# Optimization experiments

Measured on AMD Instinct MI355X. Metric: run time of the kernel, lower is better.

Reference implementation:

```python
import jax, jax.numpy as jnp
import numpy as np

DIM, EMBED, HEADS = 768, 512, 8
HEAD_DIM = EMBED // HEADS


def setup_inputs() -> dict:
    key = jax.random.key(0)
    ks = jax.random.split(key, 11)
    B, S = 4, 2048
    s = 0.02
    return {
        "query": jax.random.normal(ks[0], (B, S, DIM), jnp.float32),
        "key": jax.random.normal(ks[1], (B, S, DIM), jnp.float32),
        "value": jax.random.normal(ks[2], (B, S, DIM), jnp.float32),
        "wq": jax.random.normal(ks[3], (DIM, EMBED), jnp.float32) * s,
        "bq": jnp.zeros((EMBED,), jnp.float32),
        "wk": jax.random.normal(ks[4], (DIM, EMBED), jnp.float32) * s,
        "bk": jnp.zeros((EMBED,), jnp.float32),
        "wv": jax.random.normal(ks[5], (DIM, EMBED), jnp.float32) * s,
        "bv": jnp.zeros((EMBED,), jnp.float32),
        "wo": jax.random.normal(ks[6], (EMBED, DIM), jnp.float32) * s,
        "bo": jnp.zeros((DIM,), jnp.float32),
    }


def reference(query, key, value, wq, bq, wk, bk, wv, bv, wo, bo):
    B, S, _ = query.shape
    # QKV projections -> [B, H, S, Dh]
    def split_heads(x):
        return x.reshape(B, -1, HEADS, HEAD_DIM).transpose(0, 2, 1, 3)
    q = split_heads(query @ wq + bq)
    k = split_heads(key @ wk + bk)
    v = split_heads(value @ wv + bv)
    scores = jnp.einsum("bhqd,bhkd->bhqk", q, k) / jnp.sqrt(jnp.float32(HEAD_DIM))
    p = jax.nn.softmax(scores, axis=-1)
    x = jnp.einsum("bhqk,bhkd->bhqd", p, v)
    x = x.transpose(0, 2, 1, 3).reshape(B, S, EMBED)
    return x @ wo + bo
```

## Files before the change

### kernel.cpp

```cpp
#include <hip/hip_runtime.h>
#include <math.h>

#define NH   8
#define HD   64
#define BS   4
#define SEQL 2048
#define DIMX 768
#define EMB  512
#define MROWS (BS*SEQL)
#define NSPLIT 2
#define KSPAN (SEQL/NSPLIT)

typedef __attribute__((ext_vector_type(4))) float          f32x4;
typedef __attribute__((ext_vector_type(8))) __bf16         bf16x8;
typedef __attribute__((ext_vector_type(8))) unsigned short u16x8;
typedef __attribute__((ext_vector_type(4))) unsigned short u16x4;

union BF8 { u16x8 u; bf16x8 b; };

__device__ __forceinline__ unsigned short f2bf(float x) {
    unsigned int u = __float_as_uint(x);
    u += 0x7FFFu + ((u >> 16) & 1u);
    return (unsigned short)(u >> 16);
}

#if __has_builtin(__builtin_amdgcn_exp2f)
#define EXP2F(x) __builtin_amdgcn_exp2f(x)
#else
#define EXP2F(x) exp2f(x)
#endif

__device__ __forceinline__ bf16x8 ldb8(const unsigned short* p) {
    return *(const bf16x8*)p;
}

__global__ __launch_bounds__(256)
void cast3(const float* __restrict__ q, const float* __restrict__ k,
           const float* __restrict__ v, unsigned short* __restrict__ out)
{
    const float* src = blockIdx.y == 0 ? q : (blockIdx.y == 1 ? k : v);
    unsigned short* dst = out + (size_t)blockIdx.y * (MROWS * DIMX);
    const int n4 = MROWS * DIMX / 4;
    for (int i = blockIdx.x * 256 + threadIdx.x; i < n4; i += gridDim.x * 256) {
        f32x4 x = ((const f32x4*)src)[i];
        u16x4 o;
        o[0] = f2bf(x[0]); o[1] = f2bf(x[1]); o[2] = f2bf(x[2]); o[3] = f2bf(x[3]);
        ((u16x4*)dst)[i] = o;
    }
}

__global__ __launch_bounds__(256)
void transpose_w4(const float* __restrict__ w0, const float* __restrict__ w1,
                  const float* __restrict__ w2, const float* __restrict__ w3,
                  unsigned short* __restrict__ o0, unsigned short* __restrict__ o1,
                  unsigned short* __restrict__ o2, unsigned short* __restrict__ o3)
{
    __shared__ float sm[32][33];
    const int which = blockIdx.y;
    const float* in; unsigned short* out; int R, C;
    if      (which == 0) { in = w0; out = o0; R = DIMX; C = EMB;  }
    else if (which == 1) { in = w1; out = o1; R = DIMX; C = EMB;  }
    else if (which == 2) { in = w2; out = o2; R = DIMX; C = EMB;  }
    else                 { in = w3; out = o3; R = EMB;  C = DIMX; }
    const int nbx = C / 32;
    const int rB = (blockIdx.x / nbx) * 32, cB = (blockIdx.x % nbx) * 32;
    const int row = threadIdx.x >> 3, c4 = (threadIdx.x & 7) * 4;
    f32x4 v = *(const f32x4*)&in[(size_t)(rB + row) * C + cB + c4];
    sm[row][c4 + 0] = v[0]; sm[row][c4 + 1] = v[1];
    sm[row][c4 + 2] = v[2]; sm[row][c4 + 3] = v[3];
    __syncthreads();
    u16x4 o;
    o[0] = f2bf(sm[c4 + 0][row]); o[1] = f2bf(sm[c4 + 1][row]);
    o[2] = f2bf(sm[c4 + 2][row]); o[3] = f2bf(sm[c4 + 3][row]);
    *(u16x4*)&out[(size_t)(cB + row) * R + rB + c4] = o;
}

template<bool DIRECT>
__device__ __forceinline__ void gemm_core(
    const unsigned short* __restrict__ A, const unsigned short* __restrict__ Bt,
    int K, int mBase, int nBase,
    unsigned short* __restrict__ smA, unsigned short* __restrict__ smB,
    f32x4 (&acc)[4][4])
{
    const int tid = threadIdx.x;
    const int lane = tid & 63, w = tid >> 6;
    const int quad = lane >> 4, lanem = lane & 15;
    const int wm = w >> 1, wn = w & 1;
    const int srow = tid >> 3, c8 = (tid & 7) * 8;

    const f32x4 z4 = {0.f, 0.f, 0.f, 0.f};
    #pragma unroll
    for (int i = 0; i < 4; ++i)
        #pragma unroll
        for (int j = 0; j < 4; ++j) acc[i][j] = z4;

    for (int k0 = 0; k0 < K; k0 += 64) {
        u16x8 va[4], vb[4];
        #pragma unroll
        for (int p = 0; p < 4; ++p) {
            va[p] = *(const u16x8*)&A[(size_t)(mBase + srow + p * 32) * K + k0 + c8];
            vb[p] = *(const u16x8*)&Bt[(size_t)(nBase + srow + p * 32) * K + k0 + c8];
        }
        __syncthreads();
        #pragma unroll
        for (int p = 0; p < 4; ++p) {
            *(u16x8*)&smA[(srow + p * 32) * 72 + c8] = va[p];
            *(u16x8*)&smB[(srow + p * 32) * 72 + c8] = vb[p];
        }
        __syncthreads();
        #pragma unroll
        for (int kk = 0; kk < 64; kk += 32) {
            bf16x8 xa[4], wb[4];
            #pragma unroll
            for (int mt = 0; mt < 4; ++mt)
                xa[mt] = ldb8(&smA[(wm * 64 + mt * 16 + lanem) * 72 + kk + quad * 8]);
            #pragma unroll
            for (int nt = 0; nt < 4; ++nt)
                wb[nt] = ldb8(&smB[(wn * 64 + nt * 16 + lanem) * 72 + kk + quad * 8]);
            if constexpr (DIRECT) {
                #pragma unroll
                for (int mt = 0; mt < 4; ++mt)
                    #pragma unroll
                    for (int nt = 0; nt < 4; ++nt)
                        acc[mt][nt] = __builtin_amdgcn_mfma_f32_16x16x32_bf16(xa[mt], wb[nt], acc[mt][nt], 0, 0, 0);
            } else {
                #pragma unroll
                for (int nt = 0; nt < 4; ++nt)
                    #pragma unroll
                    for (int mt = 0; mt < 4; ++mt)
                        acc[nt][mt] = __builtin_amdgcn_mfma_f32_16x16x32_bf16(wb[nt], xa[mt], acc[nt][mt], 0, 0, 0);
            }
        }
    }
}

__global__ __launch_bounds__(256)
void gemm_qkv(const unsigned short* __restrict__ Xc, const unsigned short* __restrict__ Wt,
              const float* __restrict__ bq, const float* __restrict__ bk,
              const float* __restrict__ bv,
              unsigned short* __restrict__ Qb, unsigned short* __restrict__ Kb,
              unsigned short* __restrict__ Vtb)
{
    __shared__ unsigned short smA[128 * 72];
    __shared__ unsigned short smB[128 * 72];
    const int z = blockIdx.z;
    const unsigned short* A  = Xc + (size_t)z * (MROWS * DIMX);
    const unsigned short* Bt = Wt + (size_t)z * (EMB * DIMX);
    const float* bias = z == 0 ? bq : (z == 1 ? bk : bv);
    const int mBase = blockIdx.y * 128, nBase = blockIdx.x * 128;

    const int tid = threadIdx.x;
    const int lane = tid & 63, w = tid >> 6;
    const int quad = lane >> 4, lanem = lane & 15;
    const int wm = w >> 1, wn = w & 1;

    f32x4 acc[4][4];
    if (z == 2) {
        gemm_core<true>(A, Bt, DIMX, mBase, nBase, smA, smB, acc);
        #pragma unroll
        for (int mt = 0; mt < 4; ++mt) {
            const int sg = mBase + wm * 64 + mt * 16 + quad * 4;
            const int b = sg >> 11, s = sg & 2047;
            #pragma unroll
            for (int nt = 0; nt < 4; ++nt) {
                const int de = nBase + wn * 64 + nt * 16 + lanem;
                const float bvv = bias[de];
                const int h = de >> 6, dh = de & 63;
                u16x4 ov;
                #pragma unroll
                for (int r = 0; r < 4; ++r) ov[r] = f2bf(acc[mt][nt][r] + bvv);
                *(u16x4*)&Vtb[((size_t)((b * NH + h) * HD + dh) << 11) + s] = ov;
            }
        }
    } else {
        gemm_core<false>(A, Bt, DIMX, mBase, nBase, smA, smB, acc);
        const float os = (z == 0) ? 0.18033688f : 1.0f;
        unsigned short* C = (z == 0) ? Qb : Kb;
        #pragma unroll
        for (int nt = 0; nt < 4; ++nt) {
            const int n0 = nBase + wn * 64 + nt * 16 + quad * 4;
            const f32x4 b4 = *(const f32x4*)&bias[n0];
            #pragma unroll
            for (int mt = 0; mt < 4; ++mt) {
                const int m = mBase + wm * 64 + mt * 16 + lanem;
                u16x4 ov;
                #pragma unroll
                for (int r = 0; r < 4; ++r) ov[r] = f2bf((acc[nt][mt][r] + b4[r]) * os);
                *(u16x4*)&C[(size_t)m * EMB + n0] = ov;
            }
        }
    }
}

__global__ __launch_bounds__(256)
void gemm_out(const unsigned short* __restrict__ Xb, const unsigned short* __restrict__ Wot,
              const float* __restrict__ bo, float* __restrict__ out)
{
    __shared__ unsigned short smA[128 * 72];
    __shared__ unsigned short smB[128 * 72];
    const int mBase = blockIdx.y * 128, nBase = blockIdx.x * 128;
    const int tid = threadIdx.x;
    const int lane = tid & 63, w = tid >> 6;
    const int quad = lane >> 4, lanem = lane & 15;
    const int wm = w >> 1, wn = w & 1;

    f32x4 acc[4][4];
    gemm_core<false>(Xb, Wot, EMB, mBase, nBase, smA, smB, acc);
    #pragma unroll
    for (int nt = 0; nt < 4; ++nt) {
        const int n0 = nBase + wn * 64 + nt * 16 + quad * 4;
        const f32x4 b4 = *(const f32x4*)&bo[n0];
        #pragma unroll
        for (int mt = 0; mt < 4; ++mt) {
            const int m = mBase + wm * 64 + mt * 16 + lanem;
            f32x4 ov = acc[nt][mt] + b4;
            *(f32x4*)&out[(size_t)m * DIMX + n0] = ov;
        }
    }
}

__global__ __launch_bounds__(256)
void attn_mfma(const unsigned short* __restrict__ Qb, const unsigned short* __restrict__ Kb,
               const unsigned short* __restrict__ Vt,
               float* __restrict__ Opart, float* __restrict__ lpart)
{
    __shared__ unsigned short smK[64 * 72];
    __shared__ unsigned short smV[64 * 72];
    __shared__ unsigned short smP[4][32 * 72];
    const int id = blockIdx.x;
    const int bh = ((id & 7) << 2) | ((id >> 3) & 3);
    const int rest = id >> 5;
    const int qb = rest & 15, sp = rest >> 4;
    const int b = bh >> 3, h = bh & 7;

    const int tid = threadIdx.x;
    const int w = tid >> 6, lane = tid & 63;
    const int quad = lane >> 4, lanem = lane & 15;

    bf16x8 aq[2][2];
    #pragma unroll
    for (int rg = 0; rg < 2; ++rg) {
        const size_t qrow = (size_t)(b * SEQL + qb * 128 + w * 32 + rg * 16 + lanem) * EMB + h * HD;
        aq[rg][0] = ldb8(&Qb[qrow + quad * 8]);
        aq[rg][1] = ldb8(&Qb[qrow + 32 + quad * 8]);
    }

    const f32x4 z4 = {0.f, 0.f, 0.f, 0.f};
    f32x4 o[4][2];
    f32x4 ls[2] = {z4, z4};
    #pragma unroll
    for (int dt = 0; dt < 4; ++dt)
        #pragma unroll
        for (int rg = 0; rg < 2; ++rg) o[dt][rg] = z4;

    BF8 ones;
    #pragma unroll
    for (int i = 0; i < 8; ++i) ones.u[i] = 0x3F80;

    const unsigned short* Kbase = Kb + (size_t)b * SEQL * EMB + h * HD;
    const unsigned short* Vbase = Vt + (size_t)bh * HD * SEQL;
    unsigned short* pW = &smP[w][0];
    const int srow = tid >> 3, c8 = (tid & 7) * 8;

    for (int t = 0; t < KSPAN / 64; ++t) {
        const int k0 = sp * KSPAN + t * 64;
        u16x8 kv[2], vv[2];
        #pragma unroll
        for (int p = 0; p < 2; ++p) {
            kv[p] = *(const u16x8*)&Kbase[(size_t)(k0 + srow + p * 32) * EMB + c8];
            vv[p] = *(const u16x8*)&Vbase[(size_t)(srow + p * 32) * SEQL + k0 + c8];
        }
        __syncthreads();
        #pragma unroll
        for (int p = 0; p < 2; ++p) {
            *(u16x8*)&smK[(srow + p * 32) * 72 + c8] = kv[p];
            *(u16x8*)&smV[(srow + p * 32) * 72 + c8] = vv[p];
        }
        __syncthreads();

        #pragma unroll
        for (int nt = 0; nt < 4; ++nt) {
            bf16x8 bk0 = ldb8(&smK[(nt * 16 + lanem) * 72 + quad * 8]);
            bf16x8 bk1 = ldb8(&smK[(nt * 16 + lanem) * 72 + 32 + quad * 8]);
            #pragma unroll
            for (int rg = 0; rg < 2; ++rg) {
                f32x4 s = __builtin_amdgcn_mfma_f32_16x16x32_bf16(bk0, aq[rg][0], z4, 0, 0, 0);
                s = __builtin_amdgcn_mfma_f32_16x16x32_bf16(bk1, aq[rg][1], s, 0, 0, 0);
                u16x4 pk;
                #pragma unroll
                for (int r = 0; r < 4; ++r)
                    pk[r] = (unsigned short)(__float_as_uint(EXP2F(s[r])) >> 16);
                *(u16x4*)&pW[(rg * 16 + lanem) * 72 + nt * 16 + quad * 4] = pk;
            }
        }
        bf16x8 pb[2][2];
        #pragma unroll
        for (int rg = 0; rg < 2; ++rg) {
            pb[rg][0] = ldb8(&pW[(rg * 16 + lanem) * 72 + quad * 8]);
            pb[rg][1] = ldb8(&pW[(rg * 16 + lanem) * 72 + 32 + quad * 8]);
        }
        #pragma unroll
        for (int dt = 0; dt < 4; ++dt) {
            bf16x8 av0 = ldb8(&smV[(dt * 16 + lanem) * 72 + quad * 8]);
            bf16x8 av1 = ldb8(&smV[(dt * 16 + lanem) * 72 + 32 + quad * 8]);
            #pragma unroll
            for (int rg = 0; rg < 2; ++rg) {
                o[dt][rg] = __builtin_amdgcn_mfma_f32_16x16x32_bf16(av0, pb[rg][0], o[dt][rg], 0, 0, 0);
                o[dt][rg] = __builtin_amdgcn_mfma_f32_16x16x32_bf16(av1, pb[rg][1], o[dt][rg], 0, 0, 0);
            }
        }
        #pragma unroll
        for (int rg = 0; rg < 2; ++rg) {
            ls[rg] = __builtin_amdgcn_mfma_f32_16x16x32_bf16(ones.b, pb[rg][0], ls[rg], 0, 0, 0);
            ls[rg] = __builtin_amdgcn_mfma_f32_16x16x32_bf16(ones.b, pb[rg][1], ls[rg], 0, 0, 0);
        }
    }

    #pragma unroll
    for (int rg = 0; rg < 2; ++rg) {
        const int qloc = qb * 128 + w * 32 + rg * 16 + lanem;
        float* orow = Opart + ((size_t)sp * 32 * SEQL + (size_t)bh * SEQL + qloc) * HD;
        #pragma unroll
        for (int dt = 0; dt < 4; ++dt)
            *(f32x4*)&orow[dt * 16 + quad * 4] = o[dt][rg];
        if (quad == 0)
            lpart[(size_t)sp * 32 * SEQL + (size_t)bh * SEQL + qloc] = ls[rg][0];
    }
}

__global__ __launch_bounds__(256)
void attn_reduce(const float* __restrict__ Opart, const float* __restrict__ lpart,
                 unsigned short* __restrict__ Xb)
{
    const int lin = blockIdx.x * 256 + threadIdx.x;
    const int d4 = (lin & 15) << 2;
    const int q = (lin >> 4) & 2047;
    const int bh = lin >> 15;
    const int b = bh >> 3, h = bh & 7;
    const size_t base = ((size_t)bh * SEQL + q) * HD + d4;
    const size_t soff = (size_t)32 * SEQL * HD;
    f32x4 o0 = *(const f32x4*)&Opart[base];
    f32x4 o1 = *(const f32x4*)&Opart[base + soff];
    const float l0 = lpart[(size_t)bh * SEQL + q];
    const float l1 = lpart[(size_t)32 * SEQL + (size_t)bh * SEQL + q];
    const float rl = 1.f / (l0 + l1);
    u16x4 ov;
    #pragma unroll
    for (int r = 0; r < 4; ++r) ov[r] = f2bf((o0[r] + o1[r]) * rl);
    *(u16x4*)&Xb[((size_t)(b * SEQL + q)) * EMB + h * HD + d4] = ov;
}

extern "C" void kernel_launch(void* const* d_in, const int* in_sizes, int n_in,
                              void* d_out, int out_size, void* d_ws, size_t ws_size,
                              hipStream_t stream) {
    (void)in_sizes; (void)n_in; (void)out_size; (void)ws_size;
    const float* query = (const float*)d_in[0];
    const float* key   = (const float*)d_in[1];
    const float* value = (const float*)d_in[2];
    const float* wq = (const float*)d_in[3];
    const float* bq = (const float*)d_in[4];
    const float* wk = (const float*)d_in[5];
    const float* bk = (const float*)d_in[6];
    const float* wv = (const float*)d_in[7];
    const float* bv = (const float*)d_in[8];
    const float* wo = (const float*)d_in[9];
    const float* bo = (const float*)d_in[10];
    float* out = (float*)d_out;

    char* ws = (char*)d_ws;
    unsigned short* castb = (unsigned short*)(ws);
    float*          Opart = (float*)(ws);
    float*          lpart = (float*)(ws + 33554432);
    unsigned short* Wt    = (unsigned short*)(ws + 37748736);
    unsigned short* Wot   = (unsigned short*)(ws + 40108032);
    unsigned short* Qbuf  = (unsigned short*)(ws + 40894464);
    unsigned short* Xbuf  = Qbuf;
    unsigned short* Kbuf  = (unsigned short*)(ws + 49283072);
    unsigned short* Vtb   = (unsigned short*)(ws + 57671680);

    const dim3 blk(256);

    transpose_w4<<<dim3(384, 4), blk, 0, stream>>>(wq, wk, wv, wo,
        Wt, Wt + (size_t)EMB * DIMX, Wt + 2 * (size_t)EMB * DIMX, Wot);
    cast3<<<dim3(1024, 3), blk, 0, stream>>>(query, key, value, castb);

    gemm_qkv<<<dim3(EMB / 128, MROWS / 128, 3), blk, 0, stream>>>(
        castb, Wt, bq, bk, bv, Qbuf, Kbuf, Vtb);

    attn_mfma<<<dim3(32 * 16 * NSPLIT), blk, 0, stream>>>(Qbuf, Kbuf, Vtb, Opart, lpart);
    attn_reduce<<<dim3(4096), blk, 0, stream>>>(Opart, lpart, Xbuf);

    gemm_out<<<dim3(DIMX / 128, MROWS / 128), blk, 0, stream>>>(Xbuf, Wot, bo, out);
}
```

Baseline: 240.6 us.

## Load K/V fragments directly from global and double queries per wave

The attention kernel no longer stages K and V tiles through shared memory with two barriers per iteration. Each wave now loads its own K and V MFMA fragments straight from global memory, relying on cache hits across the four waves. Each wave handles 64 query rows instead of 32, and the grid is halved, so every K/V fragment feeds more MFMAs. The cost is redundant global/L2 traffic across waves, higher register pressure from the larger accumulators, and fewer blocks to fill the GPU.

Measured after the change: 280.0 us. 16.4% more time.

```diff
diff --git a/kernel.cpp b/kernel.cpp
--- a/kernel.cpp
+++ b/kernel.cpp
@@ -224,34 +224,34 @@
                const unsigned short* __restrict__ Vt,
                float* __restrict__ Opart, float* __restrict__ lpart)
 {
-    __shared__ unsigned short smK[64 * 72];
-    __shared__ unsigned short smV[64 * 72];
-    __shared__ unsigned short smP[4][32 * 72];
+    __shared__ unsigned short smP[4][64 * 72];
     const int id = blockIdx.x;
     const int bh = ((id & 7) << 2) | ((id >> 3) & 3);
     const int rest = id >> 5;
-    const int qb = rest & 15, sp = rest >> 4;
+    const int qb = rest & 7, sp = rest >> 3;
     const int b = bh >> 3, h = bh & 7;
 
     const int tid = threadIdx.x;
     const int w = tid >> 6, lane = tid & 63;
     const int quad = lane >> 4, lanem = lane & 15;
 
-    bf16x8 aq[2][2];
-    #pragma unroll
-    for (int rg = 0; rg < 2; ++rg) {
-        const size_t qrow = (size_t)(b * SEQL + qb * 128 + w * 32 + rg * 16 + lanem) * EMB + h * HD;
+    bf16x8 aq[4][2];
+    #pragma unroll
+    for (int rg = 0; rg < 4; ++rg) {
+        const size_t qrow = (size_t)(b * SEQL + qb * 256 + w * 64 + rg * 16 + lanem) * EMB + h * HD;
         aq[rg][0] = ldb8(&Qb[qrow + quad * 8]);
         aq[rg][1] = ldb8(&Qb[qrow + 32 + quad * 8]);
     }
 
     const f32x4 z4 = {0.f, 0.f, 0.f, 0.f};
-    f32x4 o[4][2];
-    f32x4 ls[2] = {z4, z4};
+    f32x4 o[4][4];
+    f32x4 ls[4];
     #pragma unroll
     for (int dt = 0; dt < 4; ++dt)
         #pragma unroll
-        for (int rg = 0; rg < 2; ++rg) o[dt][rg] = z4;
+        for (int rg = 0; rg < 4; ++rg) o[dt][rg] = z4;
+    #pragma unroll
+    for (int rg = 0; rg < 4; ++rg) ls[rg] = z4;
 
     BF8 ones;
     #pragma unroll
@@ -260,32 +260,31 @@
     const unsigned short* Kbase = Kb + (size_t)b * SEQL * EMB + h * HD;
     const unsigned short* Vbase = Vt + (size_t)bh * HD * SEQL;
     unsigned short* pW = &smP[w][0];
-    const int srow = tid >> 3, c8 = (tid & 7) * 8;
 
     for (int t = 0; t < KSPAN / 64; ++t) {
         const int k0 = sp * KSPAN + t * 64;
-        u16x8 kv[2], vv[2];
-        #pragma unroll
-        for (int p = 0; p < 2; ++p) {
-            kv[p] = *(const u16x8*)&Kbase[(size_t)(k0 + srow + p * 32) * EMB + c8];
-            vv[p] = *(const u16x8*)&Vbase[(size_t)(srow + p * 32) * SEQL + k0 + c8];
-        }
-        __syncthreads();
-        #pragma unroll
-        for (int p = 0; p < 2; ++p) {
-            *(u16x8*)&smK[(srow + p * 32) * 72 + c8] = kv[p];
-            *(u16x8*)&smV[(srow + p * 32) * 72 + c8] = vv[p];
-        }
-        __syncthreads();
-
+
+        bf16x8 bk[4][2];
+        bf16x8 av[4][2];
         #pragma unroll
         for (int nt = 0; nt < 4; ++nt) {
-            bf16x8 bk0 = ldb8(&smK[(nt * 16 + lanem) * 72 + quad * 8]);
-            bf16x8 bk1 = ldb8(&smK[(nt * 16 + lanem) * 72 + 32 + quad * 8]);
-            #pragma unroll
-            for (int rg = 0; rg < 2; ++rg) {
-                f32x4 s = __builtin_amdgcn_mfma_f32_16x16x32_bf16(bk0, aq[rg][0], z4, 0, 0, 0);
-                s = __builtin_amdgcn_mfma_f32_16x16x32_bf16(bk1, aq[rg][1], s, 0, 0, 0);
+            const unsigned short* kr = &Kbase[(size_t)(k0 + nt * 16 + lanem) * EMB];
+            bk[nt][0] = ldb8(kr + quad * 8);
+            bk[nt][1] = ldb8(kr + 32 + quad * 8);
+        }
+        #pragma unroll
+        for (int dt = 0; dt < 4; ++dt) {
+            const unsigned short* vr = &Vbase[(size_t)(dt * 16 + lanem) * SEQL + k0];
+            av[dt][0] = ldb8(vr + quad * 8);
+            av[dt][1] = ldb8(vr + 32 + quad * 8);
+        }
+
+        #pragma unroll
+        for (int nt = 0; nt < 4; ++nt) {
+            #pragma unroll
+            for (int rg = 0; rg < 4; ++rg) {
+                f32x4 s = __builtin_amdgcn_mfma_f32_16x16x32_bf16(bk[nt][0], aq[rg][0], z4, 0, 0, 0);
+                s = __builtin_amdgcn_mfma_f32_16x16x32_bf16(bk[nt][1], aq[rg][1], s, 0, 0, 0);
                 u16x4 pk;
                 #pragma unroll
                 for (int r = 0; r < 4; ++r)
@@ -293,32 +292,23 @@
                 *(u16x4*)&pW[(rg * 16 + lanem) * 72 + nt * 16 + quad * 4] = pk;
             }
         }
-        bf16x8 pb[2][2];
-        #pragma unroll
-        for (int rg = 0; rg < 2; ++rg) {
-            pb[rg][0] = ldb8(&pW[(rg * 16 + lanem) * 72 + quad * 8]);
-            pb[rg][1] = ldb8(&pW[(rg * 16 + lanem) * 72 + 32 + quad * 8]);
-        }
-        #pragma unroll
-        for (int dt = 0; dt < 4; ++dt) {
-            bf16x8 av0 = ldb8(&smV[(dt * 16 + lanem) * 72 + quad * 8]);
-            bf16x8 av1 = ldb8(&smV[(dt * 16 + lanem) * 72 + 32 + quad * 8]);
-            #pragma unroll
-            for (int rg = 0; rg < 2; ++rg) {
-                o[dt][rg] = __builtin_amdgcn_mfma_f32_16x16x32_bf16(av0, pb[rg][0], o[dt][rg], 0, 0, 0);
-                o[dt][rg] = __builtin_amdgcn_mfma_f32_16x16x32_bf16(av1, pb[rg][1], o[dt][rg], 0, 0, 0);
-            }
-        }
-        #pragma unroll
-        for (int rg = 0; rg < 2; ++rg) {
-            ls[rg] = __builtin_amdgcn_mfma_f32_16x16x32_bf16(ones.b, pb[rg][0], ls[rg], 0, 0, 0);
-            ls[rg] = __builtin_amdgcn_mfma_f32_16x16x32_bf16(ones.b, pb[rg][1], ls[rg], 0, 0, 0);
-        }
-    }
-
-    #pragma unroll
-    for (int rg = 0; rg < 2; ++rg) {
-        const int qloc = qb * 128 + w * 32 + rg * 16 + lanem;
+        #pragma unroll
+        for (int rg = 0; rg < 4; ++rg) {
+            bf16x8 pb0 = ldb8(&pW[(rg * 16 + lanem) * 72 + quad * 8]);
+            bf16x8 pb1 = ldb8(&pW[(rg * 16 + lanem) * 72 + 32 + quad * 8]);
+            #pragma unroll
+            for (int dt = 0; dt < 4; ++dt) {
+                o[dt][rg] = __builtin_amdgcn_mfma_f32_16x16x32_bf16(av[dt][0], pb0, o[dt][rg], 0, 0, 0);
+                o[dt][rg] = __builtin_amdgcn_mfma_f32_16x16x32_bf16(av[dt][1], pb1, o[dt][rg], 0, 0, 0);
+            }
+            ls[rg] = __builtin_amdgcn_mfma_f32_16x16x32_bf16(ones.b, pb0, ls[rg], 0, 0, 0);
+            ls[rg] = __builtin_amdgcn_mfma_f32_16x16x32_bf16(ones.b, pb1, ls[rg], 0, 0, 0);
+        }
+    }
+
+    #pragma unroll
+    for (int rg = 0; rg < 4; ++rg) {
+        const int qloc = qb * 256 + w * 64 + rg * 16 + lanem;
         float* orow = Opart + ((size_t)sp * 32 * SEQL + (size_t)bh * SEQL + qloc) * HD;
         #pragma unroll
         for (int dt = 0; dt < 4; ++dt)
@@ -387,7 +377,7 @@
     gemm_qkv<<<dim3(EMB / 128, MROWS / 128, 3), blk, 0, stream>>>(
         castb, Wt, bq, bk, bv, Qbuf, Kbuf, Vtb);
 
-    attn_mfma<<<dim3(32 * 16 * NSPLIT), blk, 0, stream>>>(Qbuf, Kbuf, Vtb, Opart, lpart);
+    attn_mfma<<<dim3(32 * 8 * NSPLIT), blk, 0, stream>>>(Qbuf, Kbuf, Vtb, Opart, lpart);
     attn_reduce<<<dim3(4096), blk, 0, stream>>>(Opart, lpart, Xbuf);
 
     gemm_out<<<dim3(DIMX / 128, MROWS / 128), blk, 0, stream>>>(Xbuf, Wot, bo, out);
```
